# Performance work log

Hardware: AMD Instinct MI355X
Metric: run time of the kernel (lower is better)

## Reference

```python
import jax, jax.numpy as jnp
import numpy as np

H = 1024
B, S = 8, 2048
EPS = 1e-5


def _layernorm(x, w, b):
    m = jnp.mean(x, axis=-1, keepdims=True)
    v = jnp.mean((x - m) ** 2, axis=-1, keepdims=True)
    return (x - m) * jax.lax.rsqrt(v + EPS) * w + b


def setup_inputs() -> dict:
    key = jax.random.key(0)
    ks = jax.random.split(key, 10)
    x = jax.random.normal(ks[0], (B, S, H), dtype=jnp.float32)
    # LayerNorm params (torch default init: weight=1, bias=0)
    qn_w = jnp.ones((H,), jnp.float32)
    qn_b = jnp.zeros((H,), jnp.float32)
    kvn_w = jnp.ones((H,), jnp.float32)
    kvn_b = jnp.zeros((H,), jnp.float32)
    # q_prime/k_prime/v_prime ~ U(-0.5, 0.5)
    q_prime = jax.random.uniform(ks[1], (1, H), jnp.float32) - 0.5
    k_prime = jax.random.uniform(ks[2], (1, H), jnp.float32) - 0.5
    v_prime = jax.random.uniform(ks[3], (1, H), jnp.float32) - 0.5
    # Linear params, torch-style fan_in init
    lim = 1.0 / np.sqrt(H)
    qW = jax.random.uniform(ks[4], (H, H), jnp.float32, -lim, lim)
    qb = jax.random.uniform(ks[5], (H,), jnp.float32, -lim, lim)
    v1W = jax.random.uniform(ks[6], (H, H), jnp.float32, -lim, lim)
    v1b = jax.random.uniform(ks[7], (H,), jnp.float32, -lim, lim)
    v2W = jax.random.uniform(ks[8], (H, H), jnp.float32, -lim, lim)
    v2b = jax.random.uniform(ks[9], (H,), jnp.float32, -lim, lim)
    return {"x": x, "qn_w": qn_w, "qn_b": qn_b, "kvn_w": kvn_w, "kvn_b": kvn_b,
            "q_prime": q_prime, "k_prime": k_prime, "v_prime": v_prime,
            "qW": qW, "qb": qb, "v1W": v1W, "v1b": v1b, "v2W": v2W, "v2b": v2b}


def reference(x, qn_w, qn_b, kvn_w, kvn_b, q_prime, k_prime, v_prime,
              qW, qb, v1W, v1b, v2W, v2b):
    divisor = jnp.sqrt(jnp.float32(x.shape[-1]))
    xqn = _layernorm(x, qn_w, qn_b)            # [B,S,H]
    xkvn = _layernorm(x, kvn_w, kvn_b)         # [B,S,H]
    kr = xkvn * jax.nn.sigmoid(k_prime)        # [B,S,H]
    qr = (xqn @ qW.T + qb) * jax.nn.sigmoid(q_prime)  # [B,S,H]
    vp = jax.nn.sigmoid(v_prime)               # [1,H]
    gate = jax.nn.sigmoid(vp @ v1W.T + v1b) * jnp.tanh(vp @ v2W.T + v2b)  # [1,H]
    vr = xkvn * gate                           # [B,S,H]
    scores = jnp.einsum('bsh,bth->bst', qr, kr) / divisor  # [B,S,S]
    b, s, t = scores.shape
    # global softmax over flattened seq x seq matrix
    attn = jax.nn.softmax(scores.reshape(b, s * t), axis=-1).reshape(b, s, t)
    attended = jnp.einsum('bst,bth->bsh', attn, vr)
    return attended + xqn
```

## Files before the change

kernel.cpp:

```cpp
#include <hip/hip_runtime.h>
#include <stdint.h>


#define DEVI __device__ __forceinline__

typedef __bf16 bf16x8 __attribute__((ext_vector_type(8)));
typedef float  f32x4  __attribute__((ext_vector_type(4)));

typedef __attribute__((address_space(3))) uint32_t lds_u32_t;
typedef __attribute__((address_space(1))) uint32_t glb_u32_t;

DEVI uint16_t f2bf(float f) {
  union { float f; uint32_t u; } v; v.f = f;
  uint32_t r = (v.u + 0x7fffu + ((v.u >> 16) & 1u)) >> 16;
  return (uint16_t)r;
}
DEVI float bf2f(uint16_t b) {
  union { uint32_t u; float f; } v; v.u = ((uint32_t)b) << 16;
  return v.f;
}
DEVI float sigm(float x) { return 1.0f / (1.0f + __expf(-x)); }

DEVI void gl_lds16(const void* g, const void* lds_base) {
  __builtin_amdgcn_global_load_lds((glb_u32_t*)(uintptr_t)g,
                                   (lds_u32_t*)(uint32_t)(uintptr_t)lds_base,
                                   16, 0, 0);
}

DEVI void gemm_tile(const uint16_t* __restrict__ A, int lda,
                    const uint16_t* __restrict__ B, int ldb,
                    int K, uint16_t* sA, uint16_t* sB, f32x4 acc[4][4])
{
  const int tid  = threadIdx.x;
  const int lane = tid & 63;
  const int w    = tid >> 6;
  const int wr   = (w >> 1) * 64;
  const int wc   = (w & 1) * 64;
  const int r0   = tid >> 2;
  const int c0   = (((tid & 3) ^ (r0 & 3)) * 8);
  const int m16  = lane & 15;
  const int q8   = ((lane >> 4) ^ (m16 & 3)) * 8;

  for (int kt = 0; kt < K; kt += 32) {
    __syncthreads();
#pragma unroll
    for (int p = 0; p < 2; p++) {
      gl_lds16(A + (size_t)(p * 64 + r0) * lda + (kt + c0), sA + (p * 256 + w * 64) * 8);
      gl_lds16(B + (size_t)(p * 64 + r0) * ldb + (kt + c0), sB + (p * 256 + w * 64) * 8);
    }
    __syncthreads();
    bf16x8 af[4], bfv[4];
#pragma unroll
    for (int i = 0; i < 4; i++) {
      af[i]  = *(const bf16x8*)(sA + (wr + i * 16 + m16) * 32 + q8);
      bfv[i] = *(const bf16x8*)(sB + (wc + i * 16 + m16) * 32 + q8);
    }
#pragma unroll
    for (int mi = 0; mi < 4; mi++)
#pragma unroll
      for (int ni = 0; ni < 4; ni++)
        acc[mi][ni] = __builtin_amdgcn_mfma_f32_16x16x32_bf16(af[mi], bfv[ni], acc[mi][ni], 0, 0, 0);
  }
}

__global__ void gate_kernel(const float* __restrict__ v_prime,
                            const float* __restrict__ v1W, const float* __restrict__ v1b,
                            const float* __restrict__ v2W, const float* __restrict__ v2b,
                            float* __restrict__ gate)
{
  const int tid = threadIdx.x, lane = tid & 63, w = tid >> 6;
  const int j = blockIdx.x * 4 + w;
  float d1 = 0.f, d2 = 0.f;
  for (int it = 0; it < 16; it++) {
    int i = it * 64 + lane;
    float vp = sigm(v_prime[i]);
    d1 += vp * v1W[(size_t)j * 1024 + i];
    d2 += vp * v2W[(size_t)j * 1024 + i];
  }
  for (int off = 32; off; off >>= 1) { d1 += __shfl_xor(d1, off); d2 += __shfl_xor(d2, off); }
  if (lane == 0) gate[j] = sigm(d1 + v1b[j]) * tanhf(d2 + v2b[j]);
}

__global__ void cvt_kernel(const float* __restrict__ src, uint16_t* __restrict__ dst)
{
  size_t i = ((size_t)blockIdx.x * 256 + threadIdx.x) * 4;
  float4 v = *(const float4*)(src + i);
  *(ushort4*)(dst + i) = make_ushort4(f2bf(v.x), f2bf(v.y), f2bf(v.z), f2bf(v.w));
}

__global__ __launch_bounds__(256) void ln_kernel(
    const float* __restrict__ x,
    const float* __restrict__ qn_w, const float* __restrict__ qn_b,
    const float* __restrict__ kvn_w, const float* __restrict__ kvn_b,
    const float* __restrict__ k_prime, const float* __restrict__ gate,
    uint16_t* __restrict__ xqn_bf, uint16_t* __restrict__ kr,
    uint16_t* __restrict__ vr, float* __restrict__ krowsq)
{
  const int lane = threadIdx.x & 63, w = threadIdx.x >> 6;
  const int row = blockIdx.x * 4 + w;
  const float4* xr = (const float4*)(x + (size_t)row * 1024);
  float4 v[4];
  float s = 0.f, sq = 0.f;
#pragma unroll
  for (int i = 0; i < 4; i++) {
    v[i] = xr[i * 64 + lane];
    s  += v[i].x + v[i].y + v[i].z + v[i].w;
    sq += v[i].x * v[i].x + v[i].y * v[i].y + v[i].z * v[i].z + v[i].w * v[i].w;
  }
  for (int off = 32; off; off >>= 1) { s += __shfl_xor(s, off); sq += __shfl_xor(sq, off); }
  const float mean = s * (1.f / 1024.f);
  const float rstd = rsqrtf(sq * (1.f / 1024.f) - mean * mean + 1e-5f);

  float ksq = 0.f;
  const size_t o4 = (size_t)row * 256;
#pragma unroll
  for (int i = 0; i < 4; i++) {
    const int idx = i * 64 + lane;
    float4 qw = ((const float4*)qn_w)[idx],  qb4 = ((const float4*)qn_b)[idx];
    float4 kw = ((const float4*)kvn_w)[idx], kb4 = ((const float4*)kvn_b)[idx];
    float4 kp = ((const float4*)k_prime)[idx], g = ((const float4*)gate)[idx];
    float xn0 = (v[i].x - mean) * rstd, xn1 = (v[i].y - mean) * rstd;
    float xn2 = (v[i].z - mean) * rstd, xn3 = (v[i].w - mean) * rstd;
    float xq0 = xn0 * qw.x + qb4.x, xq1 = xn1 * qw.y + qb4.y;
    float xq2 = xn2 * qw.z + qb4.z, xq3 = xn3 * qw.w + qb4.w;
    float xk0 = xn0 * kw.x + kb4.x, xk1 = xn1 * kw.y + kb4.y;
    float xk2 = xn2 * kw.z + kb4.z, xk3 = xn3 * kw.w + kb4.w;
    float k0 = xk0 * sigm(kp.x), k1 = xk1 * sigm(kp.y);
    float k2 = xk2 * sigm(kp.z), k3 = xk3 * sigm(kp.w);
    ksq += k0 * k0 + k1 * k1 + k2 * k2 + k3 * k3;
    ((ushort4*)xqn_bf)[o4 + idx] = make_ushort4(f2bf(xq0), f2bf(xq1), f2bf(xq2), f2bf(xq3));
    ((ushort4*)kr)[o4 + idx] = make_ushort4(f2bf(k0), f2bf(k1), f2bf(k2), f2bf(k3));
    ((ushort4*)vr)[o4 + idx] = make_ushort4(f2bf(xk0 * g.x), f2bf(xk1 * g.y),
                                            f2bf(xk2 * g.z), f2bf(xk3 * g.w));
  }
  for (int off = 32; off; off >>= 1) ksq += __shfl_xor(ksq, off);
  if (lane == 0) krowsq[row] = ksq;
}

__global__ __launch_bounds__(256) void qr_gemm_kernel(
    const uint16_t* __restrict__ xqn_bf, const uint16_t* __restrict__ qWbf,
    const float* __restrict__ qb, const float* __restrict__ q_prime,
    uint16_t* __restrict__ qr, float* __restrict__ qnormsq)
{
  __shared__ uint16_t sA[128 * 32], sB[128 * 32];
  f32x4 acc[4][4];
#pragma unroll
  for (int i = 0; i < 4; i++)
#pragma unroll
    for (int j = 0; j < 4; j++) acc[i][j] = (f32x4)0.0f;

  const int rowBase = blockIdx.y * 128, colBase = blockIdx.x * 128;
  gemm_tile(xqn_bf + (size_t)rowBase * 1024, 1024,
            qWbf + (size_t)colBase * 1024, 1024, 1024, sA, sB, acc);

  const int lane = threadIdx.x & 63, w = threadIdx.x >> 6;
  const int wr = (w >> 1) * 64, wc = (w & 1) * 64;
  float rsq[4][4] = {};
#pragma unroll
  for (int ni = 0; ni < 4; ni++) {
    int gc = colBase + wc + ni * 16 + (lane & 15);
    float scale = sigm(q_prime[gc]);
    float bias = qb[gc];
#pragma unroll
    for (int mi = 0; mi < 4; mi++)
#pragma unroll
      for (int r = 0; r < 4; r++) {
        int gr = rowBase + wr + mi * 16 + (lane >> 4) * 4 + r;
        float val = (acc[mi][ni][r] + bias) * scale;
        qr[(size_t)gr * 1024 + gc] = f2bf(val);
        rsq[mi][r] += val * val;
      }
  }
#pragma unroll
  for (int mi = 0; mi < 4; mi++)
#pragma unroll
    for (int r = 0; r < 4; r++) {
      float t = rsq[mi][r];
      t += __shfl_xor(t, 1); t += __shfl_xor(t, 2);
      t += __shfl_xor(t, 4); t += __shfl_xor(t, 8);
      rsq[mi][r] = t;
    }
  if ((lane & 15) == 0) {
#pragma unroll
    for (int mi = 0; mi < 4; mi++)
#pragma unroll
      for (int r = 0; r < 4; r++)
        atomicAdd(&qnormsq[rowBase + wr + mi * 16 + (lane >> 4) * 4 + r], rsq[mi][r]);
  }
}

__global__ void bound_kernel(const float* __restrict__ qnormsq,
                             const float* __restrict__ krowsq, float* __restrict__ MZ)
{
  const int b = blockIdx.x, tid = threadIdx.x, lane = tid & 63, w = tid >> 6;
  float mq = 0.f, mk = 0.f;
  for (int i = tid; i < 2048; i += 256) {
    mq = fmaxf(mq, qnormsq[b * 2048 + i]);
    mk = fmaxf(mk, krowsq[b * 2048 + i]);
  }
  for (int off = 32; off; off >>= 1) {
    mq = fmaxf(mq, __shfl_xor(mq, off));
    mk = fmaxf(mk, __shfl_xor(mk, off));
  }
  __shared__ float rm[4], rk[4];
  if (lane == 0) { rm[w] = mq; rk[w] = mk; }
  __syncthreads();
  if (tid == 0) {
    float qmax = fmaxf(fmaxf(rm[0], rm[1]), fmaxf(rm[2], rm[3]));
    float kmax = fmaxf(fmaxf(rk[0], rk[1]), fmaxf(rk[2], rk[3]));
    MZ[b] = sqrtf(qmax * kmax) * 0.03125f;
  }
}

__global__ void transpose_kernel(const uint16_t* __restrict__ vr, uint16_t* __restrict__ vrt)
{
  __shared__ uint16_t t[64 * 72];
  const int b = blockIdx.z;
  const int t0 = blockIdx.x * 64, h0 = blockIdx.y * 64;
  const uint16_t* src = vr + (size_t)b * 2048 * 1024;
#pragma unroll
  for (int p = 0; p < 2; p++) {
    int flat = p * 256 + threadIdx.x;
    int r = flat >> 3, c = (flat & 7) * 8;
    *(uint4*)(&t[r * 72 + c]) = *(const uint4*)(src + (size_t)(t0 + r) * 1024 + h0 + c);
  }
  __syncthreads();
  uint16_t* dst = vrt + (size_t)b * 1024 * 2048;
#pragma unroll
  for (int p = 0; p < 2; p++) {
    int flat = p * 256 + threadIdx.x;
    int oh = flat >> 3, oc = (flat & 7) * 8;
    union { uint16_t e[8]; uint4 v; } u;
#pragma unroll
    for (int j = 0; j < 8; j++) u.e[j] = t[(oc + j) * 72 + oh];
    *(uint4*)(dst + (size_t)(h0 + oh) * 2048 + t0 + oc) = u.v;
  }
}

__global__ __launch_bounds__(256) void scores_kernel(
    const uint16_t* __restrict__ qr, const uint16_t* __restrict__ kr,
    const float* __restrict__ MZ,
    uint16_t* __restrict__ scores, float* __restrict__ blockZ)
{
  __shared__ uint16_t sA[128 * 32], sB[128 * 32];
  __shared__ float redz[4];
  const int b = blockIdx.z;
  f32x4 acc[4][4];
#pragma unroll
  for (int i = 0; i < 4; i++)
#pragma unroll
    for (int j = 0; j < 4; j++) acc[i][j] = (f32x4)0.0f;

  const uint16_t* A = qr + (size_t)b * 2048 * 1024 + (size_t)blockIdx.y * 128 * 1024;
  const uint16_t* B = kr + (size_t)b * 2048 * 1024 + (size_t)blockIdx.x * 128 * 1024;
  gemm_tile(A, 1024, B, 1024, 1024, sA, sB, acc);

  const float Mhat = MZ[b];
  const int lane = threadIdx.x & 63, w = threadIdx.x >> 6;
  const int wr = (w >> 1) * 64, wc = (w & 1) * 64;
  uint16_t* S = scores + ((size_t)b << 22);
  const int rb = blockIdx.y * 128 + wr, cb = blockIdx.x * 128 + wc;

  float zt = 0.f;
#pragma unroll
  for (int mi = 0; mi < 4; mi++)
#pragma unroll
    for (int ni = 0; ni < 4; ni++)
#pragma unroll
      for (int r = 0; r < 4; r++) {
        float p = __expf(acc[mi][ni][r] * 0.03125f - Mhat);
        zt += p;
        S[(size_t)(rb + mi * 16 + (lane >> 4) * 4 + r) * 2048 + (cb + ni * 16 + (lane & 15))] = f2bf(p);
      }
  for (int off = 32; off; off >>= 1) zt += __shfl_xor(zt, off);
  if (lane == 0) redz[w] = zt;
  __syncthreads();
  if (threadIdx.x == 0) {
    int bid = (blockIdx.z * gridDim.y + blockIdx.y) * gridDim.x + blockIdx.x;
    blockZ[bid] = redz[0] + redz[1] + redz[2] + redz[3];
  }
}

__global__ void zreduce_kernel(const float* __restrict__ blockZ, float* __restrict__ MZ)
{
  const int b = blockIdx.x, tid = threadIdx.x, lane = tid & 63, w = tid >> 6;
  float z = blockZ[b * 256 + tid];
  for (int off = 32; off; off >>= 1) z += __shfl_xor(z, off);
  __shared__ float rz[4];
  if (lane == 0) rz[w] = z;
  __syncthreads();
  if (tid == 0) MZ[8 + b] = rz[0] + rz[1] + rz[2] + rz[3];
}

__global__ __launch_bounds__(256) void pv_gemm_kernel(
    const uint16_t* __restrict__ P, const uint16_t* __restrict__ vrt,
    const float* __restrict__ MZ, const uint16_t* __restrict__ xqn_bf,
    float* __restrict__ out)
{
  __shared__ uint16_t sA[128 * 32], sB[128 * 32];
  const int b = blockIdx.z;
  f32x4 acc[4][4];
#pragma unroll
  for (int i = 0; i < 4; i++)
#pragma unroll
    for (int j = 0; j < 4; j++) acc[i][j] = (f32x4)0.0f;

  const uint16_t* A = P + ((size_t)b << 22) + (size_t)blockIdx.y * 128 * 2048;
  const uint16_t* B = vrt + (size_t)b * 1024 * 2048 + (size_t)blockIdx.x * 128 * 2048;
  gemm_tile(A, 2048, B, 2048, 2048, sA, sB, acc);

  const float invZ = 1.0f / MZ[8 + b];
  const int lane = threadIdx.x & 63, w = threadIdx.x >> 6;
  const int wr = (w >> 1) * 64, wc = (w & 1) * 64;
  const int rb = blockIdx.y * 128 + wr, cb = blockIdx.x * 128 + wc;
#pragma unroll
  for (int mi = 0; mi < 4; mi++)
#pragma unroll
    for (int ni = 0; ni < 4; ni++)
#pragma unroll
      for (int r = 0; r < 4; r++) {
        int gr = rb + mi * 16 + (lane >> 4) * 4 + r;
        int gc = cb + ni * 16 + (lane & 15);
        size_t o = ((size_t)b * 2048 + gr) * 1024 + gc;
        out[o] = acc[mi][ni][r] * invZ + bf2f(xqn_bf[o]);
      }
}

extern "C" void kernel_launch(void* const* d_in, const int* in_sizes, int n_in,
                              void* d_out, int out_size, void* d_ws, size_t ws_size,
                              hipStream_t stream) {
  const float* x       = (const float*)d_in[0];
  const float* qn_w    = (const float*)d_in[1];
  const float* qn_b    = (const float*)d_in[2];
  const float* kvn_w   = (const float*)d_in[3];
  const float* kvn_b   = (const float*)d_in[4];
  const float* q_prime = (const float*)d_in[5];
  const float* k_prime = (const float*)d_in[6];
  const float* v_prime = (const float*)d_in[7];
  const float* qW      = (const float*)d_in[8];
  const float* qb      = (const float*)d_in[9];
  const float* v1W     = (const float*)d_in[10];
  const float* v1b     = (const float*)d_in[11];
  const float* v2W     = (const float*)d_in[12];
  const float* v2b     = (const float*)d_in[13];
  float* out = (float*)d_out;

  const size_t BS = 16384, H = 1024;
  char* ws = (char*)d_ws;
  size_t off = 0;
  auto alloc = [&](size_t bytes) -> char* {
    char* p = ws + off;
    off = (off + bytes + 255) & ~(size_t)255;
    return p;
  };
  float*    gate    = (float*)alloc(H * 4);
  float*    MZ      = (float*)alloc(16 * 4);
  float*    blockZ  = (float*)alloc(2048 * 4);
  float*    qnormsq = (float*)alloc(16384 * 4);
  float*    krowsq  = (float*)alloc(16384 * 4);
  uint16_t* qWbf    = (uint16_t*)alloc(H * H * 2);
  uint16_t* xqn_bf  = (uint16_t*)alloc(BS * H * 2);
  uint16_t* kr      = (uint16_t*)alloc(BS * H * 2);
  char*     regionC = alloc(BS * H * 2 * 2);
  uint16_t* vr      = (uint16_t*)regionC;
  uint16_t* scores  = (uint16_t*)regionC;
  uint16_t* vrt     = (uint16_t*)alloc(BS * H * 2);
  uint16_t* qr      = (uint16_t*)alloc(BS * H * 2);

  hipMemsetAsync(qnormsq, 0, 16384 * 4, stream);
  gate_kernel<<<256, 256, 0, stream>>>(v_prime, v1W, v1b, v2W, v2b, gate);
  cvt_kernel<<<1024, 256, 0, stream>>>(qW, qWbf);
  ln_kernel<<<4096, 256, 0, stream>>>(x, qn_w, qn_b, kvn_w, kvn_b, k_prime, gate,
                                      xqn_bf, kr, vr, krowsq);
  qr_gemm_kernel<<<dim3(8, 128), 256, 0, stream>>>(xqn_bf, qWbf, qb, q_prime, qr, qnormsq);
  transpose_kernel<<<dim3(32, 16, 8), 256, 0, stream>>>(vr, vrt);
  bound_kernel<<<8, 256, 0, stream>>>(qnormsq, krowsq, MZ);
  scores_kernel<<<dim3(16, 16, 8), 256, 0, stream>>>(qr, kr, MZ, scores, blockZ);
  zreduce_kernel<<<8, 256, 0, stream>>>(blockZ, MZ);
  pv_gemm_kernel<<<dim3(8, 16, 8), 256, 0, stream>>>(scores, vrt, MZ, xqn_bf, out);
}
```

Before: 435.4 us.

## Deepen GEMM K-tile to 64, derive vr from kr, linearize grid order

The shared GEMM tile loader now stages 64-wide K slices with an 8-way XOR swizzle, which halves the number of barrier pairs per K loop and doubles LDS use per block. The layernorm kernel no longer writes vr. The transpose kernel rebuilds it from kr scaled by gate/sigmoid(k_prime), which cuts one full bf16 activation write and read. The scores and PV kernels switch to a 1D grid whose index decomposition puts row tiles innermost, aiming for better L2 reuse of the B operand. This adds a second bf16 rounding to vr and a division by sigmoid(k_prime).

```diff
diff --git a/kernel.cpp b/kernel.cpp
--- a/kernel.cpp
+++ b/kernel.cpp
@@ -36,37 +36,42 @@
   const int w    = tid >> 6;
   const int wr   = (w >> 1) * 64;
   const int wc   = (w & 1) * 64;
-  const int r0   = tid >> 2;
-  const int c0   = (((tid & 3) ^ (r0 & 3)) * 8);
+  const int r0   = tid >> 3;
+  const int c0   = (((tid & 7) ^ (r0 & 7)) * 8);
   const int m16  = lane & 15;
-  const int q8   = ((lane >> 4) ^ (m16 & 3)) * 8;
-
-  for (int kt = 0; kt < K; kt += 32) {
+  const int quad = lane >> 4;
+
+  for (int kt = 0; kt < K; kt += 64) {
     __syncthreads();
 #pragma unroll
-    for (int p = 0; p < 2; p++) {
-      gl_lds16(A + (size_t)(p * 64 + r0) * lda + (kt + c0), sA + (p * 256 + w * 64) * 8);
-      gl_lds16(B + (size_t)(p * 64 + r0) * ldb + (kt + c0), sB + (p * 256 + w * 64) * 8);
+    for (int p = 0; p < 4; p++) {
+      gl_lds16(A + (size_t)(p * 32 + r0) * lda + (kt + c0), sA + (p * 32 + w * 8) * 64);
+      gl_lds16(B + (size_t)(p * 32 + r0) * ldb + (kt + c0), sB + (p * 32 + w * 8) * 64);
     }
     __syncthreads();
-    bf16x8 af[4], bfv[4];
-#pragma unroll
-    for (int i = 0; i < 4; i++) {
-      af[i]  = *(const bf16x8*)(sA + (wr + i * 16 + m16) * 32 + q8);
-      bfv[i] = *(const bf16x8*)(sB + (wc + i * 16 + m16) * 32 + q8);
+#pragma unroll
+    for (int s = 0; s < 2; s++) {
+      bf16x8 af[4], bfv[4];
+#pragma unroll
+      for (int i = 0; i < 4; i++) {
+        const int chA = ((s * 4 + quad) ^ (m16 & 7)) * 8;
+        af[i]  = *(const bf16x8*)(sA + (wr + i * 16 + m16) * 64 + chA);
+        bfv[i] = *(const bf16x8*)(sB + (wc + i * 16 + m16) * 64 + chA);
+      }
+#pragma unroll
+      for (int mi = 0; mi < 4; mi++)
+#pragma unroll
+        for (int ni = 0; ni < 4; ni++)
+          acc[mi][ni] = __builtin_amdgcn_mfma_f32_16x16x32_bf16(af[mi], bfv[ni], acc[mi][ni], 0, 0, 0);
     }
-#pragma unroll
-    for (int mi = 0; mi < 4; mi++)
-#pragma unroll
-      for (int ni = 0; ni < 4; ni++)
-        acc[mi][ni] = __builtin_amdgcn_mfma_f32_16x16x32_bf16(af[mi], bfv[ni], acc[mi][ni], 0, 0, 0);
   }
 }
 
 __global__ void gate_kernel(const float* __restrict__ v_prime,
                             const float* __restrict__ v1W, const float* __restrict__ v1b,
                             const float* __restrict__ v2W, const float* __restrict__ v2b,
-                            float* __restrict__ gate)
+                            const float* __restrict__ k_prime,
+                            float* __restrict__ gate2)
 {
   const int tid = threadIdx.x, lane = tid & 63, w = tid >> 6;
   const int j = blockIdx.x * 4 + w;
@@ -78,7 +83,8 @@
     d2 += vp * v2W[(size_t)j * 1024 + i];
   }
   for (int off = 32; off; off >>= 1) { d1 += __shfl_xor(d1, off); d2 += __shfl_xor(d2, off); }
-  if (lane == 0) gate[j] = sigm(d1 + v1b[j]) * tanhf(d2 + v2b[j]);
+  if (lane == 0)
+    gate2[j] = sigm(d1 + v1b[j]) * tanhf(d2 + v2b[j]) / sigm(k_prime[j]);
 }
 
 __global__ void cvt_kernel(const float* __restrict__ src, uint16_t* __restrict__ dst)
@@ -92,9 +98,9 @@
     const float* __restrict__ x,
     const float* __restrict__ qn_w, const float* __restrict__ qn_b,
     const float* __restrict__ kvn_w, const float* __restrict__ kvn_b,
-    const float* __restrict__ k_prime, const float* __restrict__ gate,
+    const float* __restrict__ k_prime,
     uint16_t* __restrict__ xqn_bf, uint16_t* __restrict__ kr,
-    uint16_t* __restrict__ vr, float* __restrict__ krowsq)
+    float* __restrict__ krowsq)
 {
   const int lane = threadIdx.x & 63, w = threadIdx.x >> 6;
   const int row = blockIdx.x * 4 + w;
@@ -118,7 +124,7 @@
     const int idx = i * 64 + lane;
     float4 qw = ((const float4*)qn_w)[idx],  qb4 = ((const float4*)qn_b)[idx];
     float4 kw = ((const float4*)kvn_w)[idx], kb4 = ((const float4*)kvn_b)[idx];
-    float4 kp = ((const float4*)k_prime)[idx], g = ((const float4*)gate)[idx];
+    float4 kp = ((const float4*)k_prime)[idx];
     float xn0 = (v[i].x - mean) * rstd, xn1 = (v[i].y - mean) * rstd;
     float xn2 = (v[i].z - mean) * rstd, xn3 = (v[i].w - mean) * rstd;
     float xq0 = xn0 * qw.x + qb4.x, xq1 = xn1 * qw.y + qb4.y;
@@ -130,8 +136,6 @@
     ksq += k0 * k0 + k1 * k1 + k2 * k2 + k3 * k3;
     ((ushort4*)xqn_bf)[o4 + idx] = make_ushort4(f2bf(xq0), f2bf(xq1), f2bf(xq2), f2bf(xq3));
     ((ushort4*)kr)[o4 + idx] = make_ushort4(f2bf(k0), f2bf(k1), f2bf(k2), f2bf(k3));
-    ((ushort4*)vr)[o4 + idx] = make_ushort4(f2bf(xk0 * g.x), f2bf(xk1 * g.y),
-                                            f2bf(xk2 * g.z), f2bf(xk3 * g.w));
   }
   for (int off = 32; off; off >>= 1) ksq += __shfl_xor(ksq, off);
   if (lane == 0) krowsq[row] = ksq;
@@ -142,7 +146,7 @@
     const float* __restrict__ qb, const float* __restrict__ q_prime,
     uint16_t* __restrict__ qr, float* __restrict__ qnormsq)
 {
-  __shared__ uint16_t sA[128 * 32], sB[128 * 32];
+  __shared__ uint16_t sA[128 * 64], sB[128 * 64];
   f32x4 acc[4][4];
 #pragma unroll
   for (int i = 0; i < 4; i++)
@@ -212,12 +216,14 @@
   }
 }
 
-__global__ void transpose_kernel(const uint16_t* __restrict__ vr, uint16_t* __restrict__ vrt)
+__global__ void transpose_kernel(const uint16_t* __restrict__ kr,
+                                 const float* __restrict__ gate2,
+                                 uint16_t* __restrict__ vrt)
 {
   __shared__ uint16_t t[64 * 72];
   const int b = blockIdx.z;
   const int t0 = blockIdx.x * 64, h0 = blockIdx.y * 64;
-  const uint16_t* src = vr + (size_t)b * 2048 * 1024;
+  const uint16_t* src = kr + (size_t)b * 2048 * 1024;
 #pragma unroll
   for (int p = 0; p < 2; p++) {
     int flat = p * 256 + threadIdx.x;
@@ -230,9 +236,10 @@
   for (int p = 0; p < 2; p++) {
     int flat = p * 256 + threadIdx.x;
     int oh = flat >> 3, oc = (flat & 7) * 8;
+    const float g = gate2[h0 + oh];
     union { uint16_t e[8]; uint4 v; } u;
 #pragma unroll
-    for (int j = 0; j < 8; j++) u.e[j] = t[(oc + j) * 72 + oh];
+    for (int j = 0; j < 8; j++) u.e[j] = f2bf(bf2f(t[(oc + j) * 72 + oh]) * g);
     *(uint4*)(dst + (size_t)(h0 + oh) * 2048 + t0 + oc) = u.v;
   }
 }
@@ -242,24 +249,25 @@
     const float* __restrict__ MZ,
     uint16_t* __restrict__ scores, float* __restrict__ blockZ)
 {
-  __shared__ uint16_t sA[128 * 32], sB[128 * 32];
+  __shared__ uint16_t sA[128 * 64], sB[128 * 64];
   __shared__ float redz[4];
-  const int b = blockIdx.z;
+  const int lid = blockIdx.x;
+  const int b = lid >> 8, c = (lid >> 4) & 15, r = lid & 15;
   f32x4 acc[4][4];
 #pragma unroll
   for (int i = 0; i < 4; i++)
 #pragma unroll
     for (int j = 0; j < 4; j++) acc[i][j] = (f32x4)0.0f;
 
-  const uint16_t* A = qr + (size_t)b * 2048 * 1024 + (size_t)blockIdx.y * 128 * 1024;
-  const uint16_t* B = kr + (size_t)b * 2048 * 1024 + (size_t)blockIdx.x * 128 * 1024;
+  const uint16_t* A = qr + (size_t)b * 2048 * 1024 + (size_t)r * 128 * 1024;
+  const uint16_t* B = kr + (size_t)b * 2048 * 1024 + (size_t)c * 128 * 1024;
   gemm_tile(A, 1024, B, 1024, 1024, sA, sB, acc);
 
   const float Mhat = MZ[b];
   const int lane = threadIdx.x & 63, w = threadIdx.x >> 6;
   const int wr = (w >> 1) * 64, wc = (w & 1) * 64;
   uint16_t* S = scores + ((size_t)b << 22);
-  const int rb = blockIdx.y * 128 + wr, cb = blockIdx.x * 128 + wc;
+  const int rb = r * 128 + wr, cb = c * 128 + wc;
 
   float zt = 0.f;
 #pragma unroll
@@ -267,18 +275,15 @@
 #pragma unroll
     for (int ni = 0; ni < 4; ni++)
 #pragma unroll
-      for (int r = 0; r < 4; r++) {
-        float p = __expf(acc[mi][ni][r] * 0.03125f - Mhat);
+      for (int rr = 0; rr < 4; rr++) {
+        float p = __expf(acc[mi][ni][rr] * 0.03125f - Mhat);
         zt += p;
-        S[(size_t)(rb + mi * 16 + (lane >> 4) * 4 + r) * 2048 + (cb + ni * 16 + (lane & 15))] = f2bf(p);
+        S[(size_t)(rb + mi * 16 + (lane >> 4) * 4 + rr) * 2048 + (cb + ni * 16 + (lane & 15))] = f2bf(p);
       }
   for (int off = 32; off; off >>= 1) zt += __shfl_xor(zt, off);
   if (lane == 0) redz[w] = zt;
   __syncthreads();
-  if (threadIdx.x == 0) {
-    int bid = (blockIdx.z * gridDim.y + blockIdx.y) * gridDim.x + blockIdx.x;
-    blockZ[bid] = redz[0] + redz[1] + redz[2] + redz[3];
-  }
+  if (threadIdx.x == 0) blockZ[lid] = redz[0] + redz[1] + redz[2] + redz[3];
 }
 
 __global__ void zreduce_kernel(const float* __restrict__ blockZ, float* __restrict__ MZ)
@@ -297,32 +302,33 @@
     const float* __restrict__ MZ, const uint16_t* __restrict__ xqn_bf,
     float* __restrict__ out)
 {
-  __shared__ uint16_t sA[128 * 32], sB[128 * 32];
-  const int b = blockIdx.z;
+  __shared__ uint16_t sA[128 * 64], sB[128 * 64];
+  const int lid = blockIdx.x;
+  const int b = lid >> 7, c = (lid >> 4) & 7, r = lid & 15;
   f32x4 acc[4][4];
 #pragma unroll
   for (int i = 0; i < 4; i++)
 #pragma unroll
     for (int j = 0; j < 4; j++) acc[i][j] = (f32x4)0.0f;
 
-  const uint16_t* A = P + ((size_t)b << 22) + (size_t)blockIdx.y * 128 * 2048;
-  const uint16_t* B = vrt + (size_t)b * 1024 * 2048 + (size_t)blockIdx.x * 128 * 2048;
+  const uint16_t* A = P + ((size_t)b << 22) + (size_t)r * 128 * 2048;
+  const uint16_t* B = vrt + (size_t)b * 1024 * 2048 + (size_t)c * 128 * 2048;
   gemm_tile(A, 2048, B, 2048, 2048, sA, sB, acc);
 
   const float invZ = 1.0f / MZ[8 + b];
   const int lane = threadIdx.x & 63, w = threadIdx.x >> 6;
   const int wr = (w >> 1) * 64, wc = (w & 1) * 64;
-  const int rb = blockIdx.y * 128 + wr, cb = blockIdx.x * 128 + wc;
+  const int rb = r * 128 + wr, cb = c * 128 + wc;
 #pragma unroll
   for (int mi = 0; mi < 4; mi++)
 #pragma unroll
     for (int ni = 0; ni < 4; ni++)
 #pragma unroll
-      for (int r = 0; r < 4; r++) {
-        int gr = rb + mi * 16 + (lane >> 4) * 4 + r;
+      for (int rr = 0; rr < 4; rr++) {
+        int gr = rb + mi * 16 + (lane >> 4) * 4 + rr;
         int gc = cb + ni * 16 + (lane & 15);
         size_t o = ((size_t)b * 2048 + gr) * 1024 + gc;
-        out[o] = acc[mi][ni][r] * invZ + bf2f(xqn_bf[o]);
+        out[o] = acc[mi][ni][rr] * invZ + bf2f(xqn_bf[o]);
       }
 }
 
@@ -353,7 +359,7 @@
     off = (off + bytes + 255) & ~(size_t)255;
     return p;
   };
-  float*    gate    = (float*)alloc(H * 4);
+  float*    gate2   = (float*)alloc(H * 4);
   float*    MZ      = (float*)alloc(16 * 4);
   float*    blockZ  = (float*)alloc(2048 * 4);
   float*    qnormsq = (float*)alloc(16384 * 4);
@@ -361,21 +367,19 @@
   uint16_t* qWbf    = (uint16_t*)alloc(H * H * 2);
   uint16_t* xqn_bf  = (uint16_t*)alloc(BS * H * 2);
   uint16_t* kr      = (uint16_t*)alloc(BS * H * 2);
-  char*     regionC = alloc(BS * H * 2 * 2);
-  uint16_t* vr      = (uint16_t*)regionC;
-  uint16_t* scores  = (uint16_t*)regionC;
+  uint16_t* scores  = (uint16_t*)alloc(BS * H * 2 * 2);
   uint16_t* vrt     = (uint16_t*)alloc(BS * H * 2);
   uint16_t* qr      = (uint16_t*)alloc(BS * H * 2);
 
   hipMemsetAsync(qnormsq, 0, 16384 * 4, stream);
-  gate_kernel<<<256, 256, 0, stream>>>(v_prime, v1W, v1b, v2W, v2b, gate);
+  gate_kernel<<<256, 256, 0, stream>>>(v_prime, v1W, v1b, v2W, v2b, k_prime, gate2);
   cvt_kernel<<<1024, 256, 0, stream>>>(qW, qWbf);
-  ln_kernel<<<4096, 256, 0, stream>>>(x, qn_w, qn_b, kvn_w, kvn_b, k_prime, gate,
-                                      xqn_bf, kr, vr, krowsq);
+  ln_kernel<<<4096, 256, 0, stream>>>(x, qn_w, qn_b, kvn_w, kvn_b, k_prime,
+                                      xqn_bf, kr, krowsq);
   qr_gemm_kernel<<<dim3(8, 128), 256, 0, stream>>>(xqn_bf, qWbf, qb, q_prime, qr, qnormsq);
-  transpose_kernel<<<dim3(32, 16, 8), 256, 0, stream>>>(vr, vrt);
+  transpose_kernel<<<dim3(32, 16, 8), 256, 0, stream>>>(kr, gate2, vrt);
   bound_kernel<<<8, 256, 0, stream>>>(qnormsq, krowsq, MZ);
-  scores_kernel<<<dim3(16, 16, 8), 256, 0, stream>>>(qr, kr, MZ, scores, blockZ);
+  scores_kernel<<<2048, 256, 0, stream>>>(qr, kr, MZ, scores, blockZ);
   zreduce_kernel<<<8, 256, 0, stream>>>(blockZ, MZ);
-  pv_gemm_kernel<<<dim3(8, 16, 8), 256, 0, stream>>>(scores, vrt, MZ, xqn_bf, out);
-}
+  pv_gemm_kernel<<<1024, 256, 0, stream>>>(scores, vrt, MZ, xqn_bf, out);
+}
```

Result: faster. 395.8 us (-9.1%).
